# Kernel tuning notes

Measured on AMD Instinct MI355X. Metric: run time of the kernel, lower is better.

## Reference

```python
import jax, jax.numpy as jnp
import numpy as np


def _bilinear_sample(img, grid, zeros_pad):
    """grid_sample, mode='bilinear', align_corners=False.
    img: [N,C,H,W]; grid: [N,H,W,2] in normalized [-1,1] (x,y order).
    zeros_pad=True -> padding_mode='zeros', else 'border'."""
    N, C, H, W = img.shape
    # unnormalize (align_corners=False): pix = (g+1)*size/2 - 0.5
    x = (grid[..., 0] + 1.0) * (W * 0.5) - 0.5
    y = (grid[..., 1] + 1.0) * (H * 0.5) - 0.5
    x0f = jnp.floor(x)
    y0f = jnp.floor(y)
    wx = (x - x0f)[..., None]
    wy = (y - y0f)[..., None]
    x0 = x0f.astype(jnp.int32)
    y0 = y0f.astype(jnp.int32)
    x1 = x0 + 1
    y1 = y0 + 1
    img_t = jnp.transpose(img, (0, 2, 3, 1))  # [N,H,W,C]
    b = jnp.arange(N)[:, None, None]

    def gather(yi, xi):
        yc = jnp.clip(yi, 0, H - 1)
        xc = jnp.clip(xi, 0, W - 1)
        v = img_t[b, yc, xc]  # [N,H,W,C]
        if zeros_pad:
            valid = (yi >= 0) & (yi < H) & (xi >= 0) & (xi < W)
            v = v * valid[..., None].astype(v.dtype)
        return v

    v00 = gather(y0, x0)
    v01 = gather(y0, x1)
    v10 = gather(y1, x0)
    v11 = gather(y1, x1)
    out = (v00 * (1 - wx) * (1 - wy) + v01 * wx * (1 - wy)
           + v10 * (1 - wx) * wy + v11 * wx * wy)
    return jnp.transpose(out, (0, 3, 1, 2))  # [N,C,H,W]


def _sample_grid(flow_curr):
    """flow_curr: [N,2,H,W] -> wrapped sample grid [N,H,W,2]."""
    N, _, H, W = flow_curr.shape
    dt = flow_curr.dtype
    gy = ((jnp.arange(H, dtype=dt) + 0.5) * (2.0 / H) - 1.0)
    gx = ((jnp.arange(W, dtype=dt) + 0.5) * (2.0 / W) - 1.0)
    base = jnp.stack(jnp.meshgrid(gx, gy, indexing='xy'), axis=-1)  # [H,W,2] (x,y)
    grid = base[None] + jnp.transpose(flow_curr, (0, 2, 3, 1))  # [N,H,W,2]
    gx_w = jnp.remainder(grid[..., 0] + 1.0, 2.0) - 1.0  # wrap x around
    return jnp.stack([gx_w, grid[..., 1]], axis=-1)


def _pscan(flows, images):
    B, L, _, H, W = flows.shape
    C = images.shape[2]
    step = 1
    while step < L:
        Lp = L - step
        fp = flows[:, :-step].reshape(B * Lp, 2, H, W)
        ip = images[:, :-step].reshape(B * Lp, C, H, W)
        fc = flows[:, step:].reshape(B * Lp, 2, H, W)
        ic = images[:, step:].reshape(B * Lp, C, H, W)
        grid = _sample_grid(fc)  # shared for flow + image sampling
        new_f = fc + _bilinear_sample(fp, grid, zeros_pad=False)  # border pad
        new_i = ic + _bilinear_sample(ip, grid, zeros_pad=True)   # zeros pad
        flows = jnp.concatenate(
            [flows[:, :step], new_f.reshape(B, Lp, 2, H, W)], axis=1)
        images = jnp.concatenate(
            [images[:, :step], new_i.reshape(B, Lp, C, H, W)], axis=1)
        step *= 2
    return images


def setup_inputs() -> dict:
    key = jax.random.key(0)
    k1, k2 = jax.random.split(key)
    B, L, C, H, W = 4, 32, 16, 128, 128
    flows = jax.random.normal(k1, (B, L, 2, H, W), dtype=jnp.float32) * 0.05
    images = jax.random.normal(k2, (B, L, C, H, W), dtype=jnp.float32)
    return {"flows": flows, "images": images}


def reference(flows, images):
    return _pscan(flows, images)
```

## Files before the change

### kernel.cpp

```cpp
#include <hip/hip_runtime.h>


constexpr int Bn = 4, Ln = 32, Cn = 16, Hn = 128, Wn = 128;
constexpr int HWp = Hn * Wn;
constexpr int FLOW_ELEMS = Bn * Ln * 2 * HWp;
constexpr int IMG_ELEMS  = Bn * Ln * Cn * HWp;
constexpr int TOTAL_PIX  = Bn * Ln * HWp;
constexpr int PX_PER_BLK = 64;
constexpr int NBLK = TOTAL_PIX / PX_PER_BLK;
constexpr int NXCD = 8, CHUNK = NBLK / NXCD;

template<bool IN_NCHW, bool OUT_NCHW, bool FLOW_NCHW, bool NEED_FLOW>
__global__ __launch_bounds__(256)
void pscan_pass(const float* __restrict__ flowIn,
                const float* __restrict__ imgIn,
                float* __restrict__ flowOut,
                float* __restrict__ imgOut,
                int step)
{
    const int n    = (blockIdx.x & (NXCD - 1)) * CHUNK + (blockIdx.x >> 3);
    const int t    = threadIdx.x;
    const int quad = t & 3;
    const int pxl  = t >> 2;
    const int P    = n * PX_PER_BLK + pxl;
    const int b    = P >> 19;
    const int l    = (P >> 14) & 31;
    const int pix  = P & (HWp - 1);
    const int h    = pix >> 7, w = pix & 127;

    const size_t fframe = (size_t)(b * Ln + l) * (2 * HWp);
    const size_t iframe = (size_t)(b * Ln + l) * (Cn * HWp);

    float fcx, fcy;
    if (FLOW_NCHW) {
        fcx = flowIn[fframe + pix];
        fcy = flowIn[fframe + HWp + pix];
    } else {
        const float2 fc = *(const float2*)&flowIn[fframe + 2 * (size_t)pix];
        fcx = fc.x; fcy = fc.y;
    }

    float4 cur;
    if (IN_NCHW) {
        const int c0 = quad * 4;
        cur.x = imgIn[iframe + (size_t)(c0 + 0) * HWp + pix];
        cur.y = imgIn[iframe + (size_t)(c0 + 1) * HWp + pix];
        cur.z = imgIn[iframe + (size_t)(c0 + 2) * HWp + pix];
        cur.w = imgIn[iframe + (size_t)(c0 + 3) * HWp + pix];
    } else {
        cur = *(const float4*)&imgIn[iframe + (size_t)pix * Cn + quad * 4];
    }

    float4 outv = cur;
    float2 outf = make_float2(fcx, fcy);

    if (l >= step) {
        float gx = (w + 0.5f) * (2.0f / Wn) - 1.0f + fcx;
        float gy = (h + 0.5f) * (2.0f / Hn) - 1.0f + fcy;
        float tt = gx + 1.0f;
        float r  = fmodf(tt, 2.0f);
        if (r < 0.0f) r += 2.0f;
        const float gxw = r - 1.0f;

        const float x = (gxw + 1.0f) * (Wn * 0.5f) - 0.5f;
        const float y = (gy  + 1.0f) * (Hn * 0.5f) - 0.5f;
        const float x0f = floorf(x), y0f = floorf(y);
        const float wx = x - x0f,    wy = y - y0f;
        const int x0 = (int)x0f, y0 = (int)y0f;
        const int x1 = x0 + 1,   y1 = y0 + 1;

        const int xc0 = min(max(x0, 0), Wn - 1), xc1 = min(max(x1, 0), Wn - 1);
        const int yc0 = min(max(y0, 0), Hn - 1), yc1 = min(max(y1, 0), Hn - 1);
        const int o00 = yc0 * Wn + xc0, o01 = yc0 * Wn + xc1;
        const int o10 = yc1 * Wn + xc0, o11 = yc1 * Wn + xc1;

        const float w00 = (1.0f - wx) * (1.0f - wy);
        const float w01 = wx * (1.0f - wy);
        const float w10 = (1.0f - wx) * wy;
        const float w11 = wx * wy;

        if (NEED_FLOW) {
            const size_t fprev = (size_t)(b * Ln + (l - step)) * (2 * HWp);
            float sx, sy;
            if (FLOW_NCHW) {
                const float* __restrict__ fp0 = flowIn + fprev;
                const float* __restrict__ fp1 = flowIn + fprev + HWp;
                sx = w00*fp0[o00] + w01*fp0[o01] + w10*fp0[o10] + w11*fp0[o11];
                sy = w00*fp1[o00] + w01*fp1[o01] + w10*fp1[o10] + w11*fp1[o11];
            } else {
                const float* __restrict__ fp = flowIn + fprev;
                const float2 t00 = *(const float2*)&fp[2*o00];
                const float2 t01 = *(const float2*)&fp[2*o01];
                const float2 t10 = *(const float2*)&fp[2*o10];
                const float2 t11 = *(const float2*)&fp[2*o11];
                sx = w00*t00.x + w01*t01.x + w10*t10.x + w11*t11.x;
                sy = w00*t00.y + w01*t01.y + w10*t10.y + w11*t11.y;
            }
            outf = make_float2(fcx + sx, fcy + sy);
        }

        const bool vx0 = (x0 >= 0) & (x0 < Wn);
        const bool vx1 = (x1 >= 0) & (x1 < Wn);
        const bool vy0 = (y0 >= 0) & (y0 < Hn);
        const bool vy1 = (y1 >= 0) & (y1 < Hn);
        const float m00 = (vy0 & vx0) ? w00 : 0.0f;
        const float m01 = (vy0 & vx1) ? w01 : 0.0f;
        const float m10 = (vy1 & vx0) ? w10 : 0.0f;
        const float m11 = (vy1 & vx1) ? w11 : 0.0f;

        const size_t iprev = (size_t)(b * Ln + (l - step)) * (Cn * HWp);
        const float* __restrict__ ip = imgIn + iprev;
        if (IN_NCHW) {
            const int c0 = quad * 4;
            float v[4];
            #pragma unroll
            for (int j = 0; j < 4; ++j) {
                const size_t co = (size_t)(c0 + j) * HWp;
                v[j] = m00*ip[co+o00] + m01*ip[co+o01] + m10*ip[co+o10] + m11*ip[co+o11];
            }
            outv = make_float4(cur.x + v[0], cur.y + v[1], cur.z + v[2], cur.w + v[3]);
        } else {
            const float4 t00 = *(const float4*)&ip[(size_t)o00 * Cn + quad*4];
            const float4 t01 = *(const float4*)&ip[(size_t)o01 * Cn + quad*4];
            const float4 t10 = *(const float4*)&ip[(size_t)o10 * Cn + quad*4];
            const float4 t11 = *(const float4*)&ip[(size_t)o11 * Cn + quad*4];
            outv.x = cur.x + (m00*t00.x + m01*t01.x + m10*t10.x + m11*t11.x);
            outv.y = cur.y + (m00*t00.y + m01*t01.y + m10*t10.y + m11*t11.y);
            outv.z = cur.z + (m00*t00.z + m01*t01.z + m10*t10.z + m11*t11.z);
            outv.w = cur.w + (m00*t00.w + m01*t01.w + m10*t10.w + m11*t11.w);
        }
    }

    if (NEED_FLOW) {
        if (quad == 0)
            *(float2*)&flowOut[fframe + 2 * (size_t)pix] = outf;
    }
    if (OUT_NCHW) {
        const int c0 = quad * 4;
        imgOut[iframe + (size_t)(c0 + 0) * HWp + pix] = outv.x;
        imgOut[iframe + (size_t)(c0 + 1) * HWp + pix] = outv.y;
        imgOut[iframe + (size_t)(c0 + 2) * HWp + pix] = outv.z;
        imgOut[iframe + (size_t)(c0 + 3) * HWp + pix] = outv.w;
    } else {
        *(float4*)&imgOut[iframe + (size_t)pix * Cn + quad * 4] = outv;
    }
}

extern "C" void kernel_launch(void* const* d_in, const int* in_sizes, int n_in,
                              void* d_out, int out_size, void* d_ws, size_t ws_size,
                              hipStream_t stream) {
    const float* f_in = (const float*)d_in[0];
    float* i_io       = (float*)d_in[1];
    float* i_out      = (float*)d_out;

    float* fA = (float*)d_ws;
    float* fB = fA + FLOW_ELEMS;
    float* iW = fB + FLOW_ELEMS;

    const size_t need = (size_t)(2 * FLOW_ELEMS + IMG_ELEMS) * sizeof(float);

    #define CONV pscan_pass<true , false, true , true >
    #define MID  pscan_pass<false, false, false, true >
    #define LAST pscan_pass<false, true , false, false>

    if (ws_size >= need) {
        CONV<<<NBLK, 256, 0, stream>>>(f_in, i_io, fA, iW,   32);
        MID <<<NBLK, 256, 0, stream>>>(fA,   iW,   fB, i_io,  1);
        MID <<<NBLK, 256, 0, stream>>>(fB,   i_io, fA, iW,    2);
        MID <<<NBLK, 256, 0, stream>>>(fA,   iW,   fB, i_io,  4);
        MID <<<NBLK, 256, 0, stream>>>(fB,   i_io, fA, iW,    8);
        LAST<<<NBLK, 256, 0, stream>>>(fA,   iW,   nullptr, i_out, 16);
    } else {
        CONV<<<NBLK, 256, 0, stream>>>(f_in, i_io, fA, i_out,  1);
        MID <<<NBLK, 256, 0, stream>>>(fA,   i_out, fB, i_io,  2);
        MID <<<NBLK, 256, 0, stream>>>(fB,   i_io,  fA, i_out, 4);
        MID <<<NBLK, 256, 0, stream>>>(fA,   i_out, fB, i_io,  8);
        LAST<<<NBLK, 256, 0, stream>>>(fB,   i_io,  nullptr, i_out, 16);
    }
    #undef CONV
    #undef MID
    #undef LAST
}
```

Baseline: 725.8 us.

## Tile blocks as 4x16 pixel patches, fuse conversion into first step, gate flow sampling

Each block now covers a 4x16 spatial tile of one frame instead of 64 consecutive pixels in a row, so the neighbouring bilinear gathers from adjacent rows share cache lines. The separate NCHW-to-NHWC conversion pass (step 32, which did no sampling) is removed, and the first real scan step reads NCHW input directly, cutting one full pass over memory. Flow sampling is limited to the quad==0 lane, so the other three lanes per pixel no longer issue redundant flow loads. The tiled pixel order gives up fully linear coalescing on the current-frame loads and stores.

```diff
diff --git a/kernel.cpp b/kernel.cpp
--- a/kernel.cpp
+++ b/kernel.cpp
@@ -22,14 +22,16 @@
     const int t    = threadIdx.x;
     const int quad = t & 3;
     const int pxl  = t >> 2;
-    const int P    = n * PX_PER_BLK + pxl;
-    const int b    = P >> 19;
-    const int l    = (P >> 14) & 31;
-    const int pix  = P & (HWp - 1);
-    const int h    = pix >> 7, w = pix & 127;
+    const int frame = n >> 8;
+    const int fb    = n & 255;
+    const int ty = fb >> 3, tx = fb & 7;
+    const int b = frame >> 5, l = frame & 31;
+    const int px_y = pxl >> 4, px_x = pxl & 15;
+    const int h = ty * 4 + px_y, w = tx * 16 + px_x;
+    const int pix = h * Wn + w;
 
-    const size_t fframe = (size_t)(b * Ln + l) * (2 * HWp);
-    const size_t iframe = (size_t)(b * Ln + l) * (Cn * HWp);
+    const size_t fframe = (size_t)frame * (2 * HWp);
+    const size_t iframe = (size_t)frame * (Cn * HWp);
 
     float fcx, fcy;
     if (FLOW_NCHW) {
@@ -79,7 +81,7 @@
         const float w10 = (1.0f - wx) * wy;
         const float w11 = wx * wy;
 
-        if (NEED_FLOW) {
+        if (NEED_FLOW && quad == 0) {
             const size_t fprev = (size_t)(b * Ln + (l - step)) * (2 * HWp);
             float sx, sy;
             if (FLOW_NCHW) {
@@ -131,10 +133,8 @@
         }
     }
 
-    if (NEED_FLOW) {
-        if (quad == 0)
-            *(float2*)&flowOut[fframe + 2 * (size_t)pix] = outf;
-    }
+    if (NEED_FLOW && quad == 0)
+        *(float2*)&flowOut[fframe + 2 * (size_t)pix] = outf;
     if (OUT_NCHW) {
         const int c0 = quad * 4;
         imgOut[iframe + (size_t)(c0 + 0) * HWp + pix] = outv.x;
@@ -159,25 +159,24 @@
 
     const size_t need = (size_t)(2 * FLOW_ELEMS + IMG_ELEMS) * sizeof(float);
 
-    #define CONV pscan_pass<true , false, true , true >
+    #define P1   pscan_pass<true , false, true , true >
     #define MID  pscan_pass<false, false, false, true >
     #define LAST pscan_pass<false, true , false, false>
 
     if (ws_size >= need) {
-        CONV<<<NBLK, 256, 0, stream>>>(f_in, i_io, fA, iW,   32);
-        MID <<<NBLK, 256, 0, stream>>>(fA,   iW,   fB, i_io,  1);
-        MID <<<NBLK, 256, 0, stream>>>(fB,   i_io, fA, iW,    2);
-        MID <<<NBLK, 256, 0, stream>>>(fA,   iW,   fB, i_io,  4);
-        MID <<<NBLK, 256, 0, stream>>>(fB,   i_io, fA, iW,    8);
-        LAST<<<NBLK, 256, 0, stream>>>(fA,   iW,   nullptr, i_out, 16);
+        P1  <<<NBLK, 256, 0, stream>>>(f_in, i_io, fA, iW,    1);
+        MID <<<NBLK, 256, 0, stream>>>(fA,   iW,   fB, i_io,  2);
+        MID <<<NBLK, 256, 0, stream>>>(fB,   i_io, fA, iW,    4);
+        MID <<<NBLK, 256, 0, stream>>>(fA,   iW,   fB, i_io,  8);
+        LAST<<<NBLK, 256, 0, stream>>>(fB,   i_io, nullptr, i_out, 16);
     } else {
-        CONV<<<NBLK, 256, 0, stream>>>(f_in, i_io, fA, i_out,  1);
+        P1  <<<NBLK, 256, 0, stream>>>(f_in, i_io,  fA, i_out, 1);
         MID <<<NBLK, 256, 0, stream>>>(fA,   i_out, fB, i_io,  2);
         MID <<<NBLK, 256, 0, stream>>>(fB,   i_io,  fA, i_out, 4);
         MID <<<NBLK, 256, 0, stream>>>(fA,   i_out, fB, i_io,  8);
         LAST<<<NBLK, 256, 0, stream>>>(fB,   i_io,  nullptr, i_out, 16);
     }
-    #undef CONV
+    #undef P1
     #undef MID
     #undef LAST
 }
```

After: 783.5 us. 8.0% more time.
